# Optimization experiments

Hardware: AMD Instinct MI355X
Metric: run time of the kernel (lower is better)

The kernel has to match this reference:

```python
import jax, jax.numpy as jnp
import numpy as np

N_NODES = 100000
N_EDGES = 600000
D = 128


def gcn_conv(x, W, b, src, dst, n_nodes):
    """PyG-style GCNConv: add self-loops, symmetric deg^{-1/2} normalization."""
    xw = x @ W  # [N, out]
    # degree of destination nodes, counting the added self-loop
    deg = jnp.zeros((n_nodes,), xw.dtype).at[dst].add(1.0) + 1.0
    dinv = jax.lax.rsqrt(deg)
    coef = dinv[src] * dinv[dst]  # [E]
    agg = jnp.zeros_like(xw).at[dst].add(xw[src] * coef[:, None])
    agg = agg + xw * (dinv * dinv)[:, None]  # self-loop term
    return agg + b


def setup_inputs() -> dict:
    key = jax.random.key(0)
    k = jax.random.split(key, 9)
    s = 1.0 / np.sqrt(D)
    return {
        "x": jax.random.normal(k[0], (N_NODES, D), jnp.float32),
        "edge_index_pos": jax.random.randint(k[1], (2, N_EDGES), 0, N_NODES, jnp.int64),
        "edge_index_neg": jax.random.randint(k[2], (2, N_EDGES), 0, N_NODES, jnp.int64),
        "W1": jax.random.uniform(k[3], (D, D), jnp.float32, -s, s),
        "b1": jnp.zeros((D,), jnp.float32),
        "W2": jax.random.uniform(k[4], (D, D), jnp.float32, -s, s),
        "b2": jnp.zeros((D,), jnp.float32),
        "weight": jax.random.uniform(k[5], (2 * D, D), jnp.float32, -s, s),
        "bias": jnp.zeros((D,), jnp.float32),
    }


def reference(x, edge_index_pos, edge_index_neg, W1, b1, W2, b2, weight, bias):
    n = x.shape[0]
    h1 = gcn_conv(x, W1, b1, edge_index_pos[0], edge_index_pos[1], n)  # [N, D]
    h2 = gcn_conv(x, W2, b2, edge_index_neg[0], edge_index_neg[1], n)  # [N, D]
    h = jnp.concatenate([h1, h2], axis=-1)  # [N, 2D]
    return h @ weight + bias  # [N, D]
```

## Files before the change

kernel.cpp:

```cpp
#include <hip/hip_runtime.h>

#define N_NODES 100000
#define NT (2 * N_NODES)
#define SPAD 100096
#define D 128
#define N_EDGES 600000
#define ET (2 * N_EDGES)
#define SCAN_B 256
#define NBLK2 ((NT + SCAN_B - 1) / SCAN_B)

typedef __attribute__((ext_vector_type(8))) short bf16x8;
typedef __attribute__((ext_vector_type(4))) float f32x4;

__device__ __forceinline__ unsigned short f2bf(float f) {
    union { float f; unsigned u; } v; v.f = f;
    unsigned r = (v.u + 0x7fff + ((v.u >> 16) & 1)) >> 16;
    return (unsigned short)r;
}
__device__ __forceinline__ float bf2f(unsigned short h) {
    union { unsigned u; float f; } v; v.u = ((unsigned)h) << 16;
    return v.f;
}

__device__ __forceinline__ long long load_idx(const void* e, long long i, int is32) {
    if (is32) return (long long)((const int*)e)[i];
    return ((const long long*)e)[i];
}

__global__ void detect_kernel(const unsigned long long* __restrict__ e, int* __restrict__ flag) {
    if (threadIdx.x == 0 && blockIdx.x == 0) {
        int is32 = 0;
        for (int i = 0; i < 64; ++i) {
            if (e[i] > 0xFFFFFFFFull) { is32 = 1; break; }
        }
        *flag = is32;
    }
}

__global__ void x2bf_kernel(const float* __restrict__ x, unsigned short* __restrict__ xb) {
    long long t = (long long)blockIdx.x * blockDim.x + threadIdx.x;
    if (t >= (long long)N_NODES * 32) return;
    float4 a = ((const float4*)x)[t];
    ((ushort4*)xb)[t] = make_ushort4(f2bf(a.x), f2bf(a.y), f2bf(a.z), f2bf(a.w));
}

__global__ void prep_Mt(const float* __restrict__ W1, const float* __restrict__ W2,
                        const float* __restrict__ weight, unsigned short* __restrict__ Mt) {
    int idx = blockIdx.x * blockDim.x + threadIdx.x;
    int j = idx >> 8, k = idx & 255;
    float a = 0.f;
    if (k < D) {
        for (int d = 0; d < D; ++d) a += W1[k * D + d] * weight[d * D + j];
    } else {
        for (int d = 0; d < D; ++d) a += W2[(k - D) * D + d] * weight[(D + d) * D + j];
    }
    Mt[j * 256 + k] = f2bf(a);
}

__global__ void prep_bt(const float* __restrict__ b1, const float* __restrict__ b2,
                        const float* __restrict__ weight, const float* __restrict__ bias,
                        float* __restrict__ bt) {
    int j = threadIdx.x;
    if (j >= D) return;
    float a = bias[j];
    for (int k = 0; k < D; ++k)
        a += b1[k] * weight[k * D + j] + b2[k] * weight[(D + k) * D + j];
    bt[j] = a;
}

__global__ void degree_both(const void* __restrict__ ep, const void* __restrict__ en,
                            const int* __restrict__ flag, int* __restrict__ degi) {
    int i = blockIdx.x * blockDim.x + threadIdx.x;
    if (i >= ET) return;
    int is32 = *flag;
    int conv = (i >= N_EDGES);
    const void* e = conv ? en : ep;
    int j = conv ? i - N_EDGES : i;
    long long d = load_idx(e, (long long)N_EDGES + j, is32);
    atomicAdd(&degi[conv * N_NODES + (int)d], 1);
}

__global__ void scan_pass1(const int* __restrict__ degi, int* __restrict__ bsum,
                           float* __restrict__ dinv) {
    __shared__ int sm[SCAN_B];
    int i = blockIdx.x * SCAN_B + threadIdx.x;
    int v = (i < NT) ? degi[i] : 0;
    if (i < NT) dinv[i] = rsqrtf((float)v + 1.0f);
    sm[threadIdx.x] = v;
    __syncthreads();
    for (int s = SCAN_B / 2; s > 0; s >>= 1) {
        if (threadIdx.x < s) sm[threadIdx.x] += sm[threadIdx.x + s];
        __syncthreads();
    }
    if (threadIdx.x == 0) bsum[blockIdx.x] = sm[0];
}

__global__ void scan_pass2(int* __restrict__ bsum) {
    __shared__ int sm[1024];
    int t = threadIdx.x;
    int v = (t < NBLK2) ? bsum[t] : 0;
    sm[t] = v;
    __syncthreads();
    for (int ofs = 1; ofs < 1024; ofs <<= 1) {
        int add = (t >= ofs) ? sm[t - ofs] : 0;
        __syncthreads();
        sm[t] += add;
        __syncthreads();
    }
    if (t < NBLK2) bsum[t] = sm[t] - v;
}

__global__ void scan_pass3(const int* __restrict__ degi, const int* __restrict__ bsum,
                           int* __restrict__ off) {
    __shared__ int sm[SCAN_B];
    int i = blockIdx.x * SCAN_B + threadIdx.x;
    int v = (i < NT) ? degi[i] : 0;
    sm[threadIdx.x] = v;
    __syncthreads();
    for (int ofs = 1; ofs < SCAN_B; ofs <<= 1) {
        int add = (threadIdx.x >= ofs) ? sm[threadIdx.x - ofs] : 0;
        __syncthreads();
        sm[threadIdx.x] += add;
        __syncthreads();
    }
    int excl = sm[threadIdx.x] - v + bsum[blockIdx.x];
    if (i < NT) off[i] = excl;
    if (i == NT - 1) off[NT] = excl + v;
}

__global__ void csr_fill_both(const void* __restrict__ ep, const void* __restrict__ en,
                              const int* __restrict__ flag, const int* __restrict__ off,
                              int* __restrict__ cnt, const float* __restrict__ dinv,
                              int2* __restrict__ csr) {
    int i = blockIdx.x * blockDim.x + threadIdx.x;
    if (i >= ET) return;
    int is32 = *flag;
    int conv = (i >= N_EDGES);
    const void* e = conv ? en : ep;
    int j = conv ? i - N_EDGES : i;
    int si = (int)load_idx(e, j, is32);
    int di = (int)load_idx(e, (long long)N_EDGES + j, is32);
    int g = conv * N_NODES;
    int node = g + di;
    int pos = off[node] + atomicAdd(&cnt[node], 1);
    float coef = dinv[g + si] * dinv[node];
    csr[pos] = make_int2(si, __float_as_int(coef));
}

template <int XBF>
__global__ void gather_both(const int* __restrict__ off, const int2* __restrict__ csr,
                            const void* __restrict__ xv, const float* __restrict__ dinv,
                            unsigned short* __restrict__ s) {
    long long t = (long long)blockIdx.x * blockDim.x + threadIdx.x;
    long long n = t >> 4;
    int c = (int)(t & 15);
    if (n >= NT) return;
    long long xrow = (n >= N_NODES) ? n - N_NODES : n;
    float dn = dinv[n];
    float f = dn * dn;
    float acc[8];
    if (XBF) {
        const unsigned short* xb = (const unsigned short*)xv;
        bf16x8 v = ((const bf16x8*)xb)[xrow * 16 + c];
        #pragma unroll
        for (int j = 0; j < 8; ++j) acc[j] = bf2f((unsigned short)v[j]) * f;
    } else {
        const float* x = (const float*)xv;
        float4 a = ((const float4*)x)[xrow * 32 + c * 2];
        float4 b = ((const float4*)x)[xrow * 32 + c * 2 + 1];
        acc[0] = a.x * f; acc[1] = a.y * f; acc[2] = a.z * f; acc[3] = a.w * f;
        acc[4] = b.x * f; acc[5] = b.y * f; acc[6] = b.z * f; acc[7] = b.w * f;
    }
    int e0 = off[n], e1 = off[n + 1];
    for (int e = e0; e < e1; ++e) {
        int2 sc = csr[e];
        float coef = __int_as_float(sc.y);
        if (XBF) {
            const unsigned short* xb = (const unsigned short*)xv;
            bf16x8 v = ((const bf16x8*)xb)[(long long)sc.x * 16 + c];
            #pragma unroll
            for (int j = 0; j < 8; ++j) acc[j] += coef * bf2f((unsigned short)v[j]);
        } else {
            const float* x = (const float*)xv;
            float4 a = ((const float4*)x)[(long long)sc.x * 32 + c * 2];
            float4 b = ((const float4*)x)[(long long)sc.x * 32 + c * 2 + 1];
            acc[0] += coef * a.x; acc[1] += coef * a.y; acc[2] += coef * a.z; acc[3] += coef * a.w;
            acc[4] += coef * b.x; acc[5] += coef * b.y; acc[6] += coef * b.z; acc[7] += coef * b.w;
        }
    }
    ushort4 o0 = make_ushort4(f2bf(acc[0]), f2bf(acc[1]), f2bf(acc[2]), f2bf(acc[3]));
    ushort4 o1 = make_ushort4(f2bf(acc[4]), f2bf(acc[5]), f2bf(acc[6]), f2bf(acc[7]));
    ((ushort4*)s)[n * 32 + c * 2]     = o0;
    ((ushort4*)s)[n * 32 + c * 2 + 1] = o1;
}

__global__ __launch_bounds__(512) void gemm_fused(
    const unsigned short* __restrict__ s1, const unsigned short* __restrict__ s2,
    const unsigned short* __restrict__ Mt, const float* __restrict__ bt,
    float* __restrict__ out) {
    __shared__ unsigned short mlds[128][264];
    int t = threadIdx.x;
    for (int c = t; c < 4096; c += 512) {
        int row = c >> 5;
        int kc = (c & 31) * 8;
        *(ulonglong2*)&mlds[row][kc] = *(const ulonglong2*)&Mt[row * 256 + kc];
    }
    __syncthreads();
    int wave = t >> 6, lane = t & 63;
    int r0 = blockIdx.x * 128 + wave * 16;
    long long arow = r0 + (lane & 15);
    int kofs = (lane >> 4) * 8;
    f32x4 acc[8];
    #pragma unroll
    for (int i = 0; i < 8; ++i) acc[i] = (f32x4){0.f, 0.f, 0.f, 0.f};
    #pragma unroll
    for (int ks = 0; ks < 8; ++ks) {
        const int kb = ks * 32;
        const unsigned short* srow = (kb < 128) ? (s1 + arow * D + kb)
                                                : (s2 + arow * D + (kb - 128));
        bf16x8 afrag = *(const bf16x8*)(srow + kofs);
        #pragma unroll
        for (int ct = 0; ct < 8; ++ct) {
            bf16x8 bfrag = *(const bf16x8*)&mlds[ct * 16 + (lane & 15)][kb + kofs];
            acc[ct] = __builtin_amdgcn_mfma_f32_16x16x32_bf16(afrag, bfrag, acc[ct], 0, 0, 0);
        }
    }
    int orow = r0 + (lane >> 4) * 4;
    #pragma unroll
    for (int ct = 0; ct < 8; ++ct) {
        int col = ct * 16 + (lane & 15);
        float b = bt[col];
        #pragma unroll
        for (int reg = 0; reg < 4; ++reg) {
            int row = orow + reg;
            if (row < N_NODES) out[(long long)row * D + col] = acc[ct][reg] + b;
        }
    }
}

extern "C" void kernel_launch(void* const* d_in, const int* in_sizes, int n_in,
                              void* d_out, int out_size, void* d_ws, size_t ws_size,
                              hipStream_t stream) {
    const float* x      = (const float*)d_in[0];
    const void*  e_pos  = d_in[1];
    const void*  e_neg  = d_in[2];
    const float* W1     = (const float*)d_in[3];
    const float* b1     = (const float*)d_in[4];
    const float* W2     = (const float*)d_in[5];
    const float* b2     = (const float*)d_in[6];
    const float* weight = (const float*)d_in[7];
    const float* bias   = (const float*)d_in[8];
    float* out = (float*)d_out;

    unsigned short* s  = (unsigned short*)d_ws;
    unsigned short* Mt = s + (size_t)(NT + 128) * D;
    float* bt   = (float*)(Mt + 128 * 256);
    float* dinv = bt + D;
    int*   flag = (int*)(dinv + NT);
    int*   degi = flag + 4;
    int*   cnt  = degi + NT;
    int*   off  = cnt + NT;
    int*   bsum = off + NT + 4;
    int2*  csr  = (int2*)(bsum + 1024);
    unsigned short* xb = (unsigned short*)(csr + ET);

    size_t need_bf16 = (size_t)((char*)(xb + (size_t)N_NODES * D) - (char*)d_ws);
    const int use_bf16_x = (ws_size >= need_bf16);

    unsigned short* s1 = s;
    unsigned short* s2 = s + (size_t)N_NODES * D;

    detect_kernel<<<1, 64, 0, stream>>>((const unsigned long long*)e_pos, flag);
    if (use_bf16_x) x2bf_kernel<<<12500, 256, 0, stream>>>(x, xb);
    prep_Mt<<<(128 * 256) / 256, 256, 0, stream>>>(W1, W2, weight, Mt);
    prep_bt<<<1, D, 0, stream>>>(b1, b2, weight, bias, bt);

    hipMemsetAsync(degi, 0, 2 * NT * sizeof(int), stream);
    const int egrid = (ET + 255) / 256;
    degree_both<<<egrid, 256, 0, stream>>>(e_pos, e_neg, flag, degi);
    scan_pass1<<<NBLK2, SCAN_B, 0, stream>>>(degi, bsum, dinv);
    scan_pass2<<<1, 1024, 0, stream>>>(bsum);
    scan_pass3<<<NBLK2, SCAN_B, 0, stream>>>(degi, bsum, off);
    csr_fill_both<<<egrid, 256, 0, stream>>>(e_pos, e_neg, flag, off, cnt, dinv, csr);

    const int ggrid = (NT * 16) / 256;
    if (use_bf16_x)
        gather_both<1><<<ggrid, 256, 0, stream>>>(off, csr, xb, dinv, s);
    else
        gather_both<0><<<ggrid, 256, 0, stream>>>(off, csr, x, dinv, s);

    gemm_fused<<<(SPAD / 128), 512, 0, stream>>>(s1, s2, Mt, bt, out);
}
```

Measured before the change: 248.6 us.

## Fuse neighbor gather into MFMA GEMM and reuse degree array as fill counter

The separate gather kernel and the bf16 intermediate buffer s are removed. Each GEMM wave now aggregates its own 16 rows for both convolutions directly into MFMA A fragments held in registers. The CSR fill decrements the degree array instead of incrementing a separate zeroed counter, which halves the memset. The fp32 fallback path is also dropped. In exchange, each lane now gathers 4 row chunks serially, which may lower parallelism and occupancy compared with the gather kernel's one-thread-per-16-byte-chunk mapping.

```diff
diff --git a/kernel.cpp b/kernel.cpp
--- a/kernel.cpp
+++ b/kernel.cpp
@@ -2,12 +2,12 @@
 
 #define N_NODES 100000
 #define NT (2 * N_NODES)
-#define SPAD 100096
 #define D 128
 #define N_EDGES 600000
 #define ET (2 * N_EDGES)
 #define SCAN_B 256
 #define NBLK2 ((NT + SCAN_B - 1) / SCAN_B)
+#define FBLK ((N_NODES + 127) / 128)
 
 typedef __attribute__((ext_vector_type(8))) short bf16x8;
 typedef __attribute__((ext_vector_type(4))) float f32x4;
@@ -130,7 +130,7 @@
 
 __global__ void csr_fill_both(const void* __restrict__ ep, const void* __restrict__ en,
                               const int* __restrict__ flag, const int* __restrict__ off,
-                              int* __restrict__ cnt, const float* __restrict__ dinv,
+                              int* __restrict__ degi, const float* __restrict__ dinv,
                               int2* __restrict__ csr) {
     int i = blockIdx.x * blockDim.x + threadIdx.x;
     if (i >= ET) return;
@@ -142,60 +142,14 @@
     int di = (int)load_idx(e, (long long)N_EDGES + j, is32);
     int g = conv * N_NODES;
     int node = g + di;
-    int pos = off[node] + atomicAdd(&cnt[node], 1);
+    int pos = off[node] + atomicSub(&degi[node], 1) - 1;
     float coef = dinv[g + si] * dinv[node];
     csr[pos] = make_int2(si, __float_as_int(coef));
 }
 
-template <int XBF>
-__global__ void gather_both(const int* __restrict__ off, const int2* __restrict__ csr,
-                            const void* __restrict__ xv, const float* __restrict__ dinv,
-                            unsigned short* __restrict__ s) {
-    long long t = (long long)blockIdx.x * blockDim.x + threadIdx.x;
-    long long n = t >> 4;
-    int c = (int)(t & 15);
-    if (n >= NT) return;
-    long long xrow = (n >= N_NODES) ? n - N_NODES : n;
-    float dn = dinv[n];
-    float f = dn * dn;
-    float acc[8];
-    if (XBF) {
-        const unsigned short* xb = (const unsigned short*)xv;
-        bf16x8 v = ((const bf16x8*)xb)[xrow * 16 + c];
-        #pragma unroll
-        for (int j = 0; j < 8; ++j) acc[j] = bf2f((unsigned short)v[j]) * f;
-    } else {
-        const float* x = (const float*)xv;
-        float4 a = ((const float4*)x)[xrow * 32 + c * 2];
-        float4 b = ((const float4*)x)[xrow * 32 + c * 2 + 1];
-        acc[0] = a.x * f; acc[1] = a.y * f; acc[2] = a.z * f; acc[3] = a.w * f;
-        acc[4] = b.x * f; acc[5] = b.y * f; acc[6] = b.z * f; acc[7] = b.w * f;
-    }
-    int e0 = off[n], e1 = off[n + 1];
-    for (int e = e0; e < e1; ++e) {
-        int2 sc = csr[e];
-        float coef = __int_as_float(sc.y);
-        if (XBF) {
-            const unsigned short* xb = (const unsigned short*)xv;
-            bf16x8 v = ((const bf16x8*)xb)[(long long)sc.x * 16 + c];
-            #pragma unroll
-            for (int j = 0; j < 8; ++j) acc[j] += coef * bf2f((unsigned short)v[j]);
-        } else {
-            const float* x = (const float*)xv;
-            float4 a = ((const float4*)x)[(long long)sc.x * 32 + c * 2];
-            float4 b = ((const float4*)x)[(long long)sc.x * 32 + c * 2 + 1];
-            acc[0] += coef * a.x; acc[1] += coef * a.y; acc[2] += coef * a.z; acc[3] += coef * a.w;
-            acc[4] += coef * b.x; acc[5] += coef * b.y; acc[6] += coef * b.z; acc[7] += coef * b.w;
-        }
-    }
-    ushort4 o0 = make_ushort4(f2bf(acc[0]), f2bf(acc[1]), f2bf(acc[2]), f2bf(acc[3]));
-    ushort4 o1 = make_ushort4(f2bf(acc[4]), f2bf(acc[5]), f2bf(acc[6]), f2bf(acc[7]));
-    ((ushort4*)s)[n * 32 + c * 2]     = o0;
-    ((ushort4*)s)[n * 32 + c * 2 + 1] = o1;
-}
-
-__global__ __launch_bounds__(512) void gemm_fused(
-    const unsigned short* __restrict__ s1, const unsigned short* __restrict__ s2,
+__global__ __launch_bounds__(512) void fused_gather_gemm(
+    const int* __restrict__ off, const int2* __restrict__ csr,
+    const unsigned short* __restrict__ xb, const float* __restrict__ dinv,
     const unsigned short* __restrict__ Mt, const float* __restrict__ bt,
     float* __restrict__ out) {
     __shared__ unsigned short mlds[128][264];
@@ -206,34 +160,76 @@
         *(ulonglong2*)&mlds[row][kc] = *(const ulonglong2*)&Mt[row * 256 + kc];
     }
     __syncthreads();
+
     int wave = t >> 6, lane = t & 63;
-    int r0 = blockIdx.x * 128 + wave * 16;
-    long long arow = r0 + (lane & 15);
-    int kofs = (lane >> 4) * 8;
-    f32x4 acc[8];
-    #pragma unroll
-    for (int i = 0; i < 8; ++i) acc[i] = (f32x4){0.f, 0.f, 0.f, 0.f};
+    int rl = lane & 15, q = lane >> 4;
+    int gr = blockIdx.x * 128 + wave * 16 + rl;
+    const bool valid = gr < N_NODES;
+
+    bf16x8 af[8];
+    #pragma unroll
+    for (int conv = 0; conv < 2; ++conv) {
+        float acc[4][8];
+        if (valid) {
+            int n = conv * N_NODES + gr;
+            float dn = dinv[n];
+            float f = dn * dn;
+            const unsigned short* xr = xb + (size_t)gr * D + q * 8;
+            #pragma unroll
+            for (int m = 0; m < 4; ++m) {
+                bf16x8 v = *(const bf16x8*)(xr + m * 32);
+                #pragma unroll
+                for (int j = 0; j < 8; ++j) acc[m][j] = bf2f((unsigned short)v[j]) * f;
+            }
+            int e0 = off[n], e1 = off[n + 1];
+            for (int e = e0; e < e1; ++e) {
+                int2 sc = csr[e];
+                float coef = __int_as_float(sc.y);
+                const unsigned short* xs = xb + (size_t)sc.x * D + q * 8;
+                #pragma unroll
+                for (int m = 0; m < 4; ++m) {
+                    bf16x8 v = *(const bf16x8*)(xs + m * 32);
+                    #pragma unroll
+                    for (int j = 0; j < 8; ++j) acc[m][j] += coef * bf2f((unsigned short)v[j]);
+                }
+            }
+        } else {
+            #pragma unroll
+            for (int m = 0; m < 4; ++m)
+                #pragma unroll
+                for (int j = 0; j < 8; ++j) acc[m][j] = 0.f;
+        }
+        #pragma unroll
+        for (int m = 0; m < 4; ++m) {
+            bf16x8 a;
+            #pragma unroll
+            for (int j = 0; j < 8; ++j) a[j] = (short)f2bf(acc[m][j]);
+            af[conv * 4 + m] = a;
+        }
+    }
+
+    f32x4 C[8];
+    #pragma unroll
+    for (int i = 0; i < 8; ++i) C[i] = (f32x4){0.f, 0.f, 0.f, 0.f};
     #pragma unroll
     for (int ks = 0; ks < 8; ++ks) {
-        const int kb = ks * 32;
-        const unsigned short* srow = (kb < 128) ? (s1 + arow * D + kb)
-                                                : (s2 + arow * D + (kb - 128));
-        bf16x8 afrag = *(const bf16x8*)(srow + kofs);
+        bf16x8 afr = af[ks];
         #pragma unroll
         for (int ct = 0; ct < 8; ++ct) {
-            bf16x8 bfrag = *(const bf16x8*)&mlds[ct * 16 + (lane & 15)][kb + kofs];
-            acc[ct] = __builtin_amdgcn_mfma_f32_16x16x32_bf16(afrag, bfrag, acc[ct], 0, 0, 0);
-        }
-    }
-    int orow = r0 + (lane >> 4) * 4;
+            bf16x8 bfr = *(const bf16x8*)&mlds[ct * 16 + rl][ks * 32 + q * 8];
+            C[ct] = __builtin_amdgcn_mfma_f32_16x16x32_bf16(afr, bfr, C[ct], 0, 0, 0);
+        }
+    }
+
+    int orow = blockIdx.x * 128 + wave * 16 + q * 4;
     #pragma unroll
     for (int ct = 0; ct < 8; ++ct) {
-        int col = ct * 16 + (lane & 15);
+        int col = ct * 16 + rl;
         float b = bt[col];
         #pragma unroll
         for (int reg = 0; reg < 4; ++reg) {
             int row = orow + reg;
-            if (row < N_NODES) out[(long long)row * D + col] = acc[ct][reg] + b;
+            if (row < N_NODES) out[(long long)row * D + col] = C[ct][reg] + b;
         }
     }
 }
@@ -252,42 +248,28 @@
     const float* bias   = (const float*)d_in[8];
     float* out = (float*)d_out;
 
-    unsigned short* s  = (unsigned short*)d_ws;
-    unsigned short* Mt = s + (size_t)(NT + 128) * D;
+    unsigned short* xb = (unsigned short*)d_ws;
+    unsigned short* Mt = xb + (size_t)N_NODES * D;
     float* bt   = (float*)(Mt + 128 * 256);
     float* dinv = bt + D;
     int*   flag = (int*)(dinv + NT);
     int*   degi = flag + 4;
-    int*   cnt  = degi + NT;
-    int*   off  = cnt + NT;
+    int*   off  = degi + NT;
     int*   bsum = off + NT + 4;
     int2*  csr  = (int2*)(bsum + 1024);
-    unsigned short* xb = (unsigned short*)(csr + ET);
-
-    size_t need_bf16 = (size_t)((char*)(xb + (size_t)N_NODES * D) - (char*)d_ws);
-    const int use_bf16_x = (ws_size >= need_bf16);
-
-    unsigned short* s1 = s;
-    unsigned short* s2 = s + (size_t)N_NODES * D;
 
     detect_kernel<<<1, 64, 0, stream>>>((const unsigned long long*)e_pos, flag);
-    if (use_bf16_x) x2bf_kernel<<<12500, 256, 0, stream>>>(x, xb);
+    x2bf_kernel<<<12500, 256, 0, stream>>>(x, xb);
     prep_Mt<<<(128 * 256) / 256, 256, 0, stream>>>(W1, W2, weight, Mt);
     prep_bt<<<1, D, 0, stream>>>(b1, b2, weight, bias, bt);
 
-    hipMemsetAsync(degi, 0, 2 * NT * sizeof(int), stream);
+    hipMemsetAsync(degi, 0, NT * sizeof(int), stream);
     const int egrid = (ET + 255) / 256;
     degree_both<<<egrid, 256, 0, stream>>>(e_pos, e_neg, flag, degi);
     scan_pass1<<<NBLK2, SCAN_B, 0, stream>>>(degi, bsum, dinv);
     scan_pass2<<<1, 1024, 0, stream>>>(bsum);
     scan_pass3<<<NBLK2, SCAN_B, 0, stream>>>(degi, bsum, off);
-    csr_fill_both<<<egrid, 256, 0, stream>>>(e_pos, e_neg, flag, off, cnt, dinv, csr);
-
-    const int ggrid = (NT * 16) / 256;
-    if (use_bf16_x)
-        gather_both<1><<<ggrid, 256, 0, stream>>>(off, csr, xb, dinv, s);
-    else
-        gather_both<0><<<ggrid, 256, 0, stream>>>(off, csr, x, dinv, s);
-
-    gemm_fused<<<(SPAD / 128), 512, 0, stream>>>(s1, s2, Mt, bt, out);
-}
+    csr_fill_both<<<egrid, 256, 0, stream>>>(e_pos, e_neg, flag, off, degi, dinv, csr);
+
+    fused_gather_gemm<<<FBLK, 512, 0, stream>>>(off, csr, xb, dinv, Mt, bt, out);
+}
```

New measurement: 240.6 us. 1.03x faster.
